# Kernel tuning notes

Hardware: AMD Instinct MI355X
Metric: run time of the kernel (lower is better)

## Reference

```python
import jax, jax.numpy as jnp
import numpy as np

EPS = 1e-5
K = 9
DILATION = 1

def bn(x, g, b, m, v):
    # x: (B,C,N,1), inference-mode BatchNorm2d with running stats
    sh = (1, -1, 1, 1)
    return (x - m.reshape(sh)) * (g.reshape(sh) / jnp.sqrt(v.reshape(sh) + EPS)) + b.reshape(sh)

def conv1x1(x, w, b):
    # w: (Cout, Cin), x: (B,Cin,N,1)
    return jnp.einsum('oc,bcnj->bonj', w, x) + b.reshape(1, -1, 1, 1)

def knn_idx(feat, k):
    # feat: (B,C,N) -> (B,N,k) indices of k nearest nodes (incl. self)
    xt = jnp.transpose(feat, (0, 2, 1))  # (B,N,C)
    x2 = jnp.sum(xt * xt, axis=-1)       # (B,N)
    dist = x2[:, :, None] - 2.0 * jnp.einsum('bnc,bmc->bnm', xt, xt) + x2[:, None, :]
    _, idx = jax.lax.top_k(-dist, k)
    return idx

def setup_inputs():
    key = jax.random.key(0)
    ks = jax.random.split(key, 24)
    B, C, H, W = 16, 256, 32, 32
    HID = 512
    def g(i, shape, s=1.0):
        return jax.random.normal(ks[i], shape, dtype=jnp.float32) * s
    def pos(i, shape):
        return jax.random.uniform(ks[i], shape, dtype=jnp.float32, minval=0.5, maxval=1.5)
    return {
        'x': g(0, (B, C, H, W)),
        'fc1_w': g(1, (C, C), 0.05), 'fc1_b': g(2, (C,), 0.05),
        'bn1_g': pos(3, (C,)), 'bn1_b': g(4, (C,), 0.1), 'bn1_m': g(5, (C,), 0.1), 'bn1_v': pos(6, (C,)),
        'gc_w': g(7, (HID, 2 * C), 0.05), 'gc_b': g(8, (HID,), 0.05),
        'gbn_g': pos(9, (HID,)), 'gbn_b': g(10, (HID,), 0.1), 'gbn_m': g(11, (HID,), 0.1), 'gbn_v': pos(12, (HID,)),
        'bn2_g': pos(13, (HID,)), 'bn2_b': g(14, (HID,), 0.1), 'bn2_m': g(15, (HID,), 0.1), 'bn2_v': pos(16, (HID,)),
        'fc2_w': g(17, (C, HID), 0.05), 'fc2_b': g(18, (C,), 0.05),
        'bn3_g': pos(19, (C,)), 'bn3_b': g(20, (C,), 0.1), 'bn3_m': g(21, (C,), 0.1), 'bn3_v': pos(22, (C,)),
    }

def reference(x, fc1_w, fc1_b, bn1_g, bn1_b, bn1_m, bn1_v,
              gc_w, gc_b, gbn_g, gbn_b, gbn_m, gbn_v,
              bn2_g, bn2_b, bn2_m, bn2_v,
              fc2_w, fc2_b, bn3_g, bn3_b, bn3_m, bn3_v):
    B, C, H, W = x.shape
    N = H * W
    x = x.reshape(B, C, N, 1)
    shortcut = x
    # fc1: 1x1 conv + BN
    h = bn(conv1x1(x, fc1_w, fc1_b), bn1_g, bn1_b, bn1_m, bn1_v)
    # DyGraphConv2d: dynamic dilated kNN graph over N nodes
    feat = h[..., 0]  # (B,C,N)
    idx = knn_idx(feat, K * DILATION)[:, :, ::DILATION]  # (B,N,K)
    # MRConv2d: max over neighbors of (x_j - x_i)
    x_j = jax.vmap(lambda f, i: f[:, i])(feat, idx)        # (B,C,N,K) gather
    diff_max = jnp.max(x_j - feat[:, :, :, None], axis=-1)  # (B,C,N)
    # interleave [x, max_diff] along channel dim -> (B, 2C, N, 1)
    m = jnp.stack([feat, diff_max], axis=2).reshape(B, 2 * C, N, 1)
    g = conv1x1(m, gc_w, gc_b)
    g = bn(g, gbn_g, gbn_b, gbn_m, gbn_v)  # BasicConv BN, act='None'
    # graph_conv Sequential: BN + GELU (erf, torch default)
    g = jax.nn.gelu(bn(g, bn2_g, bn2_b, bn2_m, bn2_v), approximate=False)
    # fc2 + residual (drop_path=0 -> identity)
    out = bn(conv1x1(g, fc2_w, fc2_b), bn3_g, bn3_b, bn3_m, bn3_v)
    return out + shortcut
```

## Files before the change

### kernel.cpp

```cpp
#include <hip/hip_runtime.h>
#include <hip/hip_bf16.h>
#include <stdint.h>

typedef unsigned long long u64;
typedef __hip_bfloat16 bf16;
typedef short s8v __attribute__((ext_vector_type(8)));
typedef short s4v __attribute__((ext_vector_type(4)));
typedef float f4v __attribute__((ext_vector_type(4)));

#define B_   16
#define C_   256
#define N_   1024
#define HID_ 512

__device__ __forceinline__ unsigned short f2b(float f) {
    unsigned u = __float_as_uint(f);
    unsigned r = (u + 0x7FFFu + ((u >> 16) & 1u)) >> 16;
    return (unsigned short)r;
}
__device__ __forceinline__ float b2f(unsigned short s) {
    return __uint_as_float(((unsigned)s) << 16);
}
__device__ __forceinline__ float ldIn(const void* p, long long i, int bf) {
    return bf ? b2f(((const unsigned short*)p)[i]) : ((const float*)p)[i];
}
__device__ __forceinline__ u64 shfl_xor_u64(u64 v, int m) {
    unsigned lo = (unsigned)v, hi = (unsigned)(v >> 32);
    lo = __shfl_xor(lo, m, 64);
    hi = __shfl_xor(hi, m, 64);
    return ((u64)hi << 32) | lo;
}

__global__ void prep_kernel(const void* xp,
    const void* fc1_b, const void* bn1_g, const void* bn1_b, const void* bn1_m, const void* bn1_v,
    const void* gc_b,  const void* gbn_g, const void* gbn_b, const void* gbn_m, const void* gbn_v,
    const void* bn2_g, const void* bn2_b, const void* bn2_m, const void* bn2_v,
    const void* fc2_b, const void* bn3_g, const void* bn3_b, const void* bn3_m, const void* bn3_v,
    int* flags, float* s1, float* t1, float* Sg, float* Tg, float* s3, float* t3,
    float* x2)
{
    __shared__ int sf;
    if (threadIdx.x == 0) {
        const unsigned short* u = (const unsigned short*)xp;
        int cnt = 0;
        for (int i = 0; i < 64; ++i) {
            int e = (u[2 * i] >> 7) & 0xFF;
            cnt += (e >= 87 && e <= 167);
        }
        int f = (cnt >= 48) ? 1 : 0;
        flags[0] = f;
        sf = f;
    }
    for (int i = threadIdx.x; i < B_ * N_; i += 512) x2[i] = 0.f;
    __syncthreads();
    int bf = sf;
    int i = threadIdx.x;
    if (i < 256) {
        float g = ldIn(bn1_g, i, bf), bb = ldIn(bn1_b, i, bf);
        float m = ldIn(bn1_m, i, bf), v  = ldIn(bn1_v, i, bf);
        float s = g / sqrtf(v + 1e-5f);
        s1[i] = s;
        t1[i] = (ldIn(fc1_b, i, bf) - m) * s + bb;

        float g3 = ldIn(bn3_g, i, bf), b3 = ldIn(bn3_b, i, bf);
        float m3 = ldIn(bn3_m, i, bf), v3 = ldIn(bn3_v, i, bf);
        float ss3 = g3 / sqrtf(v3 + 1e-5f);
        s3[i] = ss3;
        t3[i] = (ldIn(fc2_b, i, bf) - m3) * ss3 + b3;
    }
    if (i < 512) {
        float gg = ldIn(gbn_g, i, bf), gb = ldIn(gbn_b, i, bf);
        float gm = ldIn(gbn_m, i, bf), gv = ldIn(gbn_v, i, bf);
        float sg = gg / sqrtf(gv + 1e-5f);
        float g2 = ldIn(bn2_g, i, bf), b2 = ldIn(bn2_b, i, bf);
        float m2 = ldIn(bn2_m, i, bf), v2 = ldIn(bn2_v, i, bf);
        float s2 = g2 / sqrtf(v2 + 1e-5f);
        Sg[i] = sg * s2;
        Tg[i] = ((ldIn(gc_b, i, bf) - gm) * sg + gb - m2) * s2 + b2;
    }
}

__global__ __launch_bounds__(256)
void cast_weights(const void* w1, const void* wg, const void* w2,
                  short* W1h, short* W1l, short* Wgb, short* W2b,
                  const int* flags)
{
    int inf = flags[0];
    int i = blockIdx.x * 256 + threadIdx.x;
    if (i < 65536) {
        float f = ldIn(w1, i, inf);
        unsigned short h = f2b(f);
        W1h[i] = (short)h;
        W1l[i] = (short)f2b(f - b2f(h));
    } else if (i < 65536 + 262144) {
        int j = i - 65536;
        Wgb[j] = (short)f2b(ldIn(wg, j, inf));
    } else {
        int j = i - 327680;
        W2b[j] = (short)f2b(ldIn(w2, j, inf));
    }
}

__global__ __launch_bounds__(256)
void transpose_split_x(const void* __restrict__ X, short* __restrict__ xth,
                       short* __restrict__ xtl, const int* __restrict__ flags)
{
    __shared__ float tile[64][68];
    int inf = flags[0];
    int t = threadIdx.x;
    int n0 = blockIdx.x * 64, c0 = blockIdx.y * 64, b = blockIdx.z;

    #pragma unroll
    for (int rr = 0; rr < 4; ++rr) {
        int cl = (t >> 4) + rr * 16;
        int nl = (t & 15) * 4;
        long long g = ((long long)b * C_ + c0 + cl) * N_ + n0 + nl;
        if (inf) {
            s4v v = *(const s4v*)((const short*)X + g);
            tile[cl][nl + 0] = b2f((unsigned short)v[0]);
            tile[cl][nl + 1] = b2f((unsigned short)v[1]);
            tile[cl][nl + 2] = b2f((unsigned short)v[2]);
            tile[cl][nl + 3] = b2f((unsigned short)v[3]);
        } else {
            f4v v = *(const f4v*)((const float*)X + g);
            tile[cl][nl + 0] = v[0]; tile[cl][nl + 1] = v[1];
            tile[cl][nl + 2] = v[2]; tile[cl][nl + 3] = v[3];
        }
    }
    __syncthreads();

    int nl = t >> 2, cseg = t & 3;
    long long base = ((long long)((b << 10) + n0 + nl)) * C_ + c0 + cseg * 16;
    s8v h0, h1, l0, l1;
    #pragma unroll
    for (int cc = 0; cc < 16; ++cc) {
        float f = tile[cseg * 16 + cc][nl];
        unsigned short h = f2b(f);
        unsigned short l = f2b(f - b2f(h));
        if (cc < 8) { h0[cc] = (short)h; l0[cc] = (short)l; }
        else        { h1[cc - 8] = (short)h; l1[cc - 8] = (short)l; }
    }
    *(s8v*)(xth + base)     = h0;
    *(s8v*)(xth + base + 8) = h1;
    *(s8v*)(xtl + base)     = l0;
    *(s8v*)(xtl + base + 8) = l1;
}

__global__ __launch_bounds__(256)
void fc1_mfma(const short* __restrict__ W1h, const short* __restrict__ W1l,
              const short* __restrict__ xth, const short* __restrict__ xtl,
              const float* __restrict__ s1, const float* __restrict__ t1,
              float* __restrict__ Ft, short* __restrict__ Fhi,
              short* __restrict__ Flo, float* __restrict__ x2)
{
    __shared__ __align__(16) char ldsbuf[30720];
    short* Wh = (short*)(ldsbuf);
    short* Wl = (short*)(ldsbuf + 10240);
    short* Xh = (short*)(ldsbuf + 20480);
    short* Xl = (short*)(ldsbuf + 25600);

    int t = threadIdx.x;
    int n0 = blockIdx.x * 64, o0 = blockIdx.y * 128, b = blockIdx.z;
    int wv = t >> 6, ln15 = t & 15, quad = (t >> 4) & 3;

    f4v acc[8];
    #pragma unroll
    for (int i = 0; i < 8; ++i) acc[i] = 0.f;

    for (int kc = 0; kc < 8; ++kc) {
        __syncthreads();
        #pragma unroll
        for (int s = 0; s < 6; ++s) {
            int sid = t + s * 256;
            int row = sid >> 2, seg = sid & 3;
            const short* src;
            short* dst;
            if (row < 128)      { dst = &Wh[row * 40 + seg * 8];         src = W1h + (long long)(o0 + row) * C_; }
            else if (row < 256) { dst = &Wl[(row - 128) * 40 + seg * 8]; src = W1l + (long long)(o0 + row - 128) * C_; }
            else if (row < 320) { dst = &Xh[(row - 256) * 40 + seg * 8]; src = xth + ((long long)((b << 10) + n0 + row - 256)) * C_; }
            else                { dst = &Xl[(row - 320) * 40 + seg * 8]; src = xtl + ((long long)((b << 10) + n0 + row - 320)) * C_; }
            *(s8v*)dst = *(const s8v*)(src + kc * 32 + seg * 8);
        }
        __syncthreads();
        s8v xh8 = *(s8v*)&Xh[(wv * 16 + ln15) * 40 + quad * 8];
        s8v xl8 = *(s8v*)&Xl[(wv * 16 + ln15) * 40 + quad * 8];
        #pragma unroll
        for (int i = 0; i < 8; ++i) {
            s8v wh8 = *(s8v*)&Wh[(i * 16 + ln15) * 40 + quad * 8];
            s8v wl8 = *(s8v*)&Wl[(i * 16 + ln15) * 40 + quad * 8];
            acc[i] = __builtin_amdgcn_mfma_f32_16x16x32_bf16(wh8, xh8, acc[i], 0, 0, 0);
            acc[i] = __builtin_amdgcn_mfma_f32_16x16x32_bf16(wh8, xl8, acc[i], 0, 0, 0);
            acc[i] = __builtin_amdgcn_mfma_f32_16x16x32_bf16(wl8, xh8, acc[i], 0, 0, 0);
        }
    }

    int n = n0 + wv * 16 + ln15;
    long long nb = (long long)(b << 10) + n;
    float p2 = 0.f;
    #pragma unroll
    for (int i = 0; i < 8; ++i) {
        int ob = o0 + i * 16 + quad * 4;
        f4v f;
        s4v hi, lo;
        #pragma unroll
        for (int r = 0; r < 4; ++r) {
            float v = acc[i][r] * s1[ob + r] + t1[ob + r];
            f[r] = v;
            unsigned short h = f2b(v);
            hi[r] = (short)h;
            lo[r] = (short)f2b(v - b2f(h));
            p2 += v * v;
        }
        *(f4v*)(Ft  + nb * C_ + ob) = f;
        *(s4v*)(Fhi + nb * C_ + ob) = hi;
        *(s4v*)(Flo + nb * C_ + ob) = lo;
    }
    p2 += __shfl_xor(p2, 16, 64);
    p2 += __shfl_xor(p2, 32, 64);
    if (quad == 0) atomicAdd(&x2[nb], p2);
}

__global__ __launch_bounds__(256)
void gram_topk(const short* __restrict__ Fhi, const short* __restrict__ Flo,
               const float* __restrict__ x2, u64* __restrict__ Part)
{
    __shared__ __align__(16) char ldsbuf[31232];
    short* Ah  = (short*)(ldsbuf);
    short* Al  = (short*)(ldsbuf + 10240);
    short* Bh  = (short*)(ldsbuf + 20480);
    short* Bl  = (short*)(ldsbuf + 25600);
    float* x2s = (float*)(ldsbuf + 30720);
    u64*   mrg  = (u64*)(ldsbuf);
    u64*   mrg2 = (u64*)(ldsbuf + 20480);

    int t = threadIdx.x;
    int q0 = blockIdx.x * 64, mq = blockIdx.y, b = blockIdx.z;
    int wv = t >> 6, ln15 = t & 15, quad = (t >> 4) & 3;

    if (t < 128) x2s[t] = x2[(b << 10) + mq * 128 + t];

    f4v acc[8];
    #pragma unroll
    for (int i = 0; i < 8; ++i) acc[i] = 0.f;

    for (int kc = 0; kc < 8; ++kc) {
        __syncthreads();
        #pragma unroll
        for (int s = 0; s < 6; ++s) {
            int sid = t + s * 256;
            int row = sid >> 2, seg = sid & 3;
            const short* src;
            short* dst;
            int grow;
            if (row < 128)      { dst = &Ah[row * 40 + seg * 8];         grow = mq * 128 + row;       src = Fhi; }
            else if (row < 256) { dst = &Al[(row - 128) * 40 + seg * 8]; grow = mq * 128 + row - 128; src = Flo; }
            else if (row < 320) { dst = &Bh[(row - 256) * 40 + seg * 8]; grow = q0 + row - 256;       src = Fhi; }
            else                { dst = &Bl[(row - 320) * 40 + seg * 8]; grow = q0 + row - 320;       src = Flo; }
            *(s8v*)dst = *(const s8v*)(src + ((long long)((b << 10) + grow)) * C_ + kc * 32 + seg * 8);
        }
        __syncthreads();
        s8v qh = *(s8v*)&Bh[(wv * 16 + ln15) * 40 + quad * 8];
        s8v ql = *(s8v*)&Bl[(wv * 16 + ln15) * 40 + quad * 8];
        #pragma unroll
        for (int i = 0; i < 8; ++i) {
            s8v mh = *(s8v*)&Ah[(i * 16 + ln15) * 40 + quad * 8];
            s8v ml = *(s8v*)&Al[(i * 16 + ln15) * 40 + quad * 8];
            acc[i] = __builtin_amdgcn_mfma_f32_16x16x32_bf16(mh, qh, acc[i], 0, 0, 0);
            acc[i] = __builtin_amdgcn_mfma_f32_16x16x32_bf16(mh, ql, acc[i], 0, 0, 0);
            acc[i] = __builtin_amdgcn_mfma_f32_16x16x32_bf16(ml, qh, acc[i], 0, 0, 0);
        }
    }

    u64 l[9];
    #pragma unroll
    for (int i = 0; i < 9; ++i) l[i] = ~0ULL;
    #pragma unroll
    for (int i = 0; i < 8; ++i) {
        #pragma unroll
        for (int r = 0; r < 4; ++r) {
            int mloc = i * 16 + quad * 4 + r;
            float d = x2s[mloc] - 2.f * acc[i][r];
            unsigned u = __float_as_uint(d);
            u = (u & 0x80000000u) ? ~u : (u | 0x80000000u);
            u64 key = ((u64)u << 32) | (unsigned)(mq * 128 + mloc);
            if (key < l[8]) {
                u64 x = key;
                #pragma unroll
                for (int jj = 0; jj < 9; ++jj) {
                    u64 lo2 = l[jj] < x ? l[jj] : x;
                    u64 hi2 = l[jj] < x ? x : l[jj];
                    l[jj] = lo2; x = hi2;
                }
            }
        }
    }

    __syncthreads();
    {
        int qloc = wv * 16 + ln15;
        #pragma unroll
        for (int k = 0; k < 9; ++k) mrg[(qloc * 4 + quad) * 9 + k] = l[k];
    }
    __syncthreads();
    if (t < 128) {
        int r = t >> 1, pr = t & 1;
        const u64* LA = &mrg[(r * 4 + pr * 2) * 9];
        const u64* LB = LA + 9;
        int ia = 0, ib = 0;
        u64* Po = &mrg2[(r * 2 + pr) * 9];
        #pragma unroll
        for (int k = 0; k < 9; ++k) {
            u64 va = LA[ia], vb = LB[ib];
            bool ta = va < vb;
            Po[k] = ta ? va : vb;
            ia += ta; ib += !ta;
        }
    }
    __syncthreads();
    if (t < 64) {
        const u64* LA = &mrg2[(t * 2) * 9];
        const u64* LB = LA + 9;
        int ia = 0, ib = 0;
        u64* P = Part + (((long long)((b << 10) + q0 + t)) * 8 + mq) * 9;
        #pragma unroll
        for (int k = 0; k < 9; ++k) {
            u64 va = LA[ia], vb = LB[ib];
            bool ta = va < vb;
            P[k] = ta ? va : vb;
            ia += ta; ib += !ta;
        }
    }
}

__global__ __launch_bounds__(256)
void build_Mt(const float* __restrict__ Ft, const u64* __restrict__ Part,
              short* __restrict__ Mt)
{
    int t = threadIdx.x;
    int wv = t >> 6, lane = t & 63;
    int n = blockIdx.x * 4 + wv;
    int b = blockIdx.y;
    long long nb = (long long)(b << 10) + n;

    const u64* L = Part + nb * 72 + (long long)(lane & 7) * 9;
    u64 l[9];
    #pragma unroll
    for (int k = 0; k < 9; ++k) l[k] = L[k];
    #pragma unroll
    for (int s = 1; s <= 4; s <<= 1) {
        u64 p[9];
        #pragma unroll
        for (int k = 0; k < 9; ++k) p[k] = shfl_xor_u64(l[k], s);
        #pragma unroll
        for (int k = 0; k < 9; ++k) {
            u64 x = p[k];
            if (x < l[8]) {
                #pragma unroll
                for (int jj = 0; jj < 9; ++jj) {
                    u64 lo2 = l[jj] < x ? l[jj] : x;
                    u64 hi2 = l[jj] < x ? x : l[jj];
                    l[jj] = lo2; x = hi2;
                }
            }
        }
    }

    int c0 = lane * 4;
    f4v f = *(const f4v*)(Ft + nb * C_ + c0);
    f4v mx = {-3.4e38f, -3.4e38f, -3.4e38f, -3.4e38f};
    #pragma unroll
    for (int k = 0; k < 9; ++k) {
        int id = (int)(l[k] & 0xFFFFFFFFu);
        f4v g = *(const f4v*)(Ft + ((long long)(b << 10) + id) * C_ + c0);
        mx[0] = fmaxf(mx[0], g[0]); mx[1] = fmaxf(mx[1], g[1]);
        mx[2] = fmaxf(mx[2], g[2]); mx[3] = fmaxf(mx[3], g[3]);
    }
    s8v m8;
    #pragma unroll
    for (int r = 0; r < 4; ++r) {
        m8[2 * r]     = (short)f2b(f[r]);
        m8[2 * r + 1] = (short)f2b(mx[r] - f[r]);
    }
    *(s8v*)(Mt + nb * (2 * C_) + 2 * c0) = m8;
}

template<int EPI>
__global__ __launch_bounds__(256)
void mfma_gemm(const short* __restrict__ A, const short* __restrict__ Bm,
               void* __restrict__ Out, const float* __restrict__ scale,
               const float* __restrict__ bias, const void* __restrict__ resid,
               const int* __restrict__ flags, int K, int Odim)
{
    __shared__ __align__(16) short As[128 * 40];
    __shared__ __align__(16) short Bs[64 * 40];

    int t = threadIdx.x, b = blockIdx.z;
    int n0 = blockIdx.x * 64, o0 = blockIdx.y * 128;
    int wv = t >> 6, ln15 = t & 15, quad = (t >> 4) & 3;

    f4v acc[8];
    #pragma unroll
    for (int i = 0; i < 8; ++i) acc[i] = 0.f;

    int nkc = K >> 5;
    for (int kc = 0; kc < nkc; ++kc) {
        __syncthreads();
        #pragma unroll
        for (int s = 0; s < 3; ++s) {
            int sid = t + s * 256;
            int row = sid >> 2, seg = sid & 3;
            if (row < 128)
                *(s8v*)&As[row * 40 + seg * 8] =
                    *(const s8v*)(A + (long long)(o0 + row) * K + kc * 32 + seg * 8);
            else
                *(s8v*)&Bs[(row - 128) * 40 + seg * 8] =
                    *(const s8v*)(Bm + ((long long)((b << 10) + n0 + row - 128)) * K + kc * 32 + seg * 8);
        }
        __syncthreads();
        s8v bf = *(s8v*)&Bs[(wv * 16 + ln15) * 40 + quad * 8];
        #pragma unroll
        for (int i = 0; i < 8; ++i) {
            s8v a = *(s8v*)&As[(i * 16 + ln15) * 40 + quad * 8];
            acc[i] = __builtin_amdgcn_mfma_f32_16x16x32_bf16(a, bf, acc[i], 0, 0, 0);
        }
    }

    int inf = flags[0];
    int n = n0 + wv * 16 + ln15;
    #pragma unroll
    for (int i = 0; i < 8; ++i) {
        int ob = o0 + i * 16 + quad * 4;
        if (EPI == 0) {
            s4v g;
            #pragma unroll
            for (int r = 0; r < 4; ++r) {
                float val = acc[i][r] * scale[ob + r] + bias[ob + r];
                val = 0.5f * val * (1.0f + erff(val * 0.70710678118654752f));
                g[r] = (short)f2b(val);
            }
            *(s4v*)((short*)Out + ((long long)((b << 10) + n)) * Odim + ob) = g;
        } else {
            #pragma unroll
            for (int r = 0; r < 4; ++r) {
                int o = ob + r;
                long long oi = ((long long)b * Odim + o) * N_ + n;
                ((float*)Out)[oi] = acc[i][r] * scale[o] + bias[o] + ldIn(resid, oi, inf);
            }
        }
    }
}

extern "C" void kernel_launch(void* const* d_in, const int* in_sizes, int n_in,
                              void* d_out, int out_size, void* d_ws, size_t ws_size,
                              hipStream_t stream)
{
    const void* p[23];
    if (n_in >= 23 && in_sizes[0] != 4194304 && in_sizes[22] == 4194304) {
        const int amap[23] = {
            22, 13, 12, 1, 0, 2, 3,
            21, 20, 17, 16, 18, 19,
            5, 4, 6, 7,
            15, 14, 9, 8, 10, 11 };
        for (int i = 0; i < 23; ++i) p[i] = d_in[amap[i]];
    } else {
        for (int i = 0; i < 23; ++i) p[i] = d_in[i];
    }

    const void* x     = p[0];
    const void* fc1_w = p[1];
    const void* fc1_b = p[2];
    const void* bn1_g = p[3];
    const void* bn1_b = p[4];
    const void* bn1_m = p[5];
    const void* bn1_v = p[6];
    const void* gc_w  = p[7];
    const void* gc_b  = p[8];
    const void* gbn_g = p[9];
    const void* gbn_b = p[10];
    const void* gbn_m = p[11];
    const void* gbn_v = p[12];
    const void* bn2_g = p[13];
    const void* bn2_b = p[14];
    const void* bn2_m = p[15];
    const void* bn2_v = p[16];
    const void* fc2_w = p[17];
    const void* fc2_b = p[18];
    const void* bn3_g = p[19];
    const void* bn3_b = p[20];
    const void* bn3_m = p[21];
    const void* bn3_v = p[22];

    char* ws = (char*)d_ws;
    size_t off = 0;
    int*   flags = (int*)ws;
    float* s1 = (float*)(ws + 256);
    float* t1 = s1 + 256;
    float* s3 = t1 + 256;
    float* t3 = s3 + 256;
    float* Sg = t3 + 256;
    float* Tg = Sg + 512;
    off = 16384;
    short* W1h   = (short*)(ws + off); off += (size_t)C_ * C_ * 2;
    short* W1l   = (short*)(ws + off); off += (size_t)C_ * C_ * 2;
    short* Wgb   = (short*)(ws + off); off += (size_t)HID_ * 2 * C_ * 2;
    short* W2b   = (short*)(ws + off); off += (size_t)C_ * HID_ * 2;
    short* xth   = (short*)(ws + off); off += (size_t)B_ * N_ * C_ * 2;
    short* xtl   = (short*)(ws + off); off += (size_t)B_ * N_ * C_ * 2;
    float* Ft    = (float*)(ws + off); off += (size_t)B_ * N_ * C_ * 4;
    short* Fhi   = (short*)(ws + off); off += (size_t)B_ * N_ * C_ * 2;
    short* Flo   = (short*)(ws + off); off += (size_t)B_ * N_ * C_ * 2;
    float* x2    = (float*)(ws + off); off += (size_t)B_ * N_ * 4;
    u64*   Part  = (u64*)  (ws + off); off += (size_t)B_ * N_ * 8 * 9 * 8;
    short* Mt    = (short*)(ws + off); off += (size_t)B_ * N_ * 2 * C_ * 2;
    short* Gt    = (short*)(ws + off); off += (size_t)B_ * N_ * HID_ * 2;

    prep_kernel<<<1, 512, 0, stream>>>(x,
        fc1_b, bn1_g, bn1_b, bn1_m, bn1_v,
        gc_b, gbn_g, gbn_b, gbn_m, gbn_v,
        bn2_g, bn2_b, bn2_m, bn2_v,
        fc2_b, bn3_g, bn3_b, bn3_m, bn3_v,
        flags, s1, t1, Sg, Tg, s3, t3, x2);

    cast_weights<<<1792, 256, 0, stream>>>(fc1_w, gc_w, fc2_w,
                                           W1h, W1l, Wgb, W2b, flags);

    transpose_split_x<<<dim3(16, 4, 16), 256, 0, stream>>>(x, xth, xtl, flags);

    fc1_mfma<<<dim3(16, 2, 16), 256, 0, stream>>>(
        W1h, W1l, xth, xtl, s1, t1, Ft, Fhi, Flo, x2);

    gram_topk<<<dim3(16, 8, 16), 256, 0, stream>>>(Fhi, Flo, x2, Part);

    build_Mt<<<dim3(256, 16), 256, 0, stream>>>(Ft, Part, Mt);

    mfma_gemm<0><<<dim3(16, 4, 16), 256, 0, stream>>>(
        Wgb, Mt, Gt, Sg, Tg, nullptr, flags, 2 * C_, HID_);

    mfma_gemm<1><<<dim3(16, 2, 16), 256, 0, stream>>>(
        W2b, Gt, d_out, s3, t3, x, flags, HID_, C_);
}
```

Before: 301.9 us.

## Double-buffer weight tiles via direct global-to-LDS loads and register-resident B operand

In fc1 and gram_topk, the per-wave B operand (activation/query rows) is now loaded once from global memory into registers for all K chunks rather than being staged through LDS. The A operand (weights/candidate rows) is copied with global_load_lds straight into a double-buffered, unpadded LDS layout, and the next chunk is prefetched while MFMAs consume the current one. This removes one of the two barriers per iteration and the VGPR round-trip on the staging path, so loads can overlap compute. The costs are higher register pressure from 16 s8v registers per thread, and possible LDS bank conflicts because the row padding has been removed.

```diff
diff --git a/kernel.cpp b/kernel.cpp
--- a/kernel.cpp
+++ b/kernel.cpp
@@ -12,6 +12,11 @@
 #define C_   256
 #define N_   1024
 #define HID_ 512
+
+#define GLD16(g, l)                                                         \
+    __builtin_amdgcn_global_load_lds(                                       \
+        (const __attribute__((address_space(1))) void*)(g),                 \
+        (__attribute__((address_space(3))) void*)(l), 16, 0, 0)
 
 __device__ __forceinline__ unsigned short f2b(float f) {
     unsigned u = __float_as_uint(f);
@@ -153,46 +158,62 @@
               float* __restrict__ Ft, short* __restrict__ Fhi,
               short* __restrict__ Flo, float* __restrict__ x2)
 {
-    __shared__ __align__(16) char ldsbuf[30720];
-    short* Wh = (short*)(ldsbuf);
-    short* Wl = (short*)(ldsbuf + 10240);
-    short* Xh = (short*)(ldsbuf + 20480);
-    short* Xl = (short*)(ldsbuf + 25600);
+    __shared__ __align__(16) char ldsbuf[32768];
 
     int t = threadIdx.x;
     int n0 = blockIdx.x * 64, o0 = blockIdx.y * 128, b = blockIdx.z;
-    int wv = t >> 6, ln15 = t & 15, quad = (t >> 4) & 3;
+    int wv = t >> 6, lane = t & 63, ln15 = t & 15, quad = (t >> 4) & 3;
+
+    const short* gAh = W1h + (long long)(o0 + wv * 32 + (lane >> 2)) * C_ + (lane & 3) * 8;
+    const short* gAl = W1l + (long long)(o0 + wv * 32 + (lane >> 2)) * C_ + (lane & 3) * 8;
+    short* lH0 = (short*)(ldsbuf)           + wv * 32 * 32;
+    short* lL0 = (short*)(ldsbuf + 8192)    + wv * 32 * 32;
+    short* lH1 = (short*)(ldsbuf + 16384)   + wv * 32 * 32;
+    short* lL1 = (short*)(ldsbuf + 24576)   + wv * 32 * 32;
+
+#define FC1_STAGE(kc_, bi_) do {                                              \
+        short* dh = (bi_) ? lH1 : lH0;                                        \
+        short* dl = (bi_) ? lL1 : lL0;                                        \
+        GLD16(gAh + (kc_) * 32,            dh);                               \
+        GLD16(gAh + (kc_) * 32 + 16 * C_,  dh + 16 * 32);                     \
+        GLD16(gAl + (kc_) * 32,            dl);                               \
+        GLD16(gAl + (kc_) * 32 + 16 * C_,  dl + 16 * 32);                     \
+    } while (0)
+
+    FC1_STAGE(0, 0);
+
+    s8v xh[8], xl[8];
+    {
+        long long xoff = (long long)((b << 10) + n0 + wv * 16 + ln15) * C_ + quad * 8;
+        #pragma unroll
+        for (int kc = 0; kc < 8; ++kc) {
+            xh[kc] = *(const s8v*)(xth + xoff + kc * 32);
+            xl[kc] = *(const s8v*)(xtl + xoff + kc * 32);
+        }
+    }
 
     f4v acc[8];
     #pragma unroll
     for (int i = 0; i < 8; ++i) acc[i] = 0.f;
 
+    __syncthreads();
+
+    #pragma unroll
     for (int kc = 0; kc < 8; ++kc) {
+        if (kc < 7) FC1_STAGE(kc + 1, (kc + 1) & 1);
+        const short* Ah_c = (const short*)(ldsbuf + (kc & 1) * 16384);
+        const short* Al_c = Ah_c + 4096;
+        #pragma unroll
+        for (int i = 0; i < 8; ++i) {
+            s8v wh8 = *(const s8v*)&Ah_c[(i * 16 + ln15) * 32 + quad * 8];
+            s8v wl8 = *(const s8v*)&Al_c[(i * 16 + ln15) * 32 + quad * 8];
+            acc[i] = __builtin_amdgcn_mfma_f32_16x16x32_bf16(wh8, xh[kc], acc[i], 0, 0, 0);
+            acc[i] = __builtin_amdgcn_mfma_f32_16x16x32_bf16(wh8, xl[kc], acc[i], 0, 0, 0);
+            acc[i] = __builtin_amdgcn_mfma_f32_16x16x32_bf16(wl8, xh[kc], acc[i], 0, 0, 0);
+        }
         __syncthreads();
-        #pragma unroll
-        for (int s = 0; s < 6; ++s) {
-            int sid = t + s * 256;
-            int row = sid >> 2, seg = sid & 3;
-            const short* src;
-            short* dst;
-            if (row < 128)      { dst = &Wh[row * 40 + seg * 8];         src = W1h + (long long)(o0 + row) * C_; }
-            else if (row < 256) { dst = &Wl[(row - 128) * 40 + seg * 8]; src = W1l + (long long)(o0 + row - 128) * C_; }
-            else if (row < 320) { dst = &Xh[(row - 256) * 40 + seg * 8]; src = xth + ((long long)((b << 10) + n0 + row - 256)) * C_; }
-            else                { dst = &Xl[(row - 320) * 40 + seg * 8]; src = xtl + ((long long)((b << 10) + n0 + row - 320)) * C_; }
-            *(s8v*)dst = *(const s8v*)(src + kc * 32 + seg * 8);
-        }
-        __syncthreads();
-        s8v xh8 = *(s8v*)&Xh[(wv * 16 + ln15) * 40 + quad * 8];
-        s8v xl8 = *(s8v*)&Xl[(wv * 16 + ln15) * 40 + quad * 8];
-        #pragma unroll
-        for (int i = 0; i < 8; ++i) {
-            s8v wh8 = *(s8v*)&Wh[(i * 16 + ln15) * 40 + quad * 8];
-            s8v wl8 = *(s8v*)&Wl[(i * 16 + ln15) * 40 + quad * 8];
-            acc[i] = __builtin_amdgcn_mfma_f32_16x16x32_bf16(wh8, xh8, acc[i], 0, 0, 0);
-            acc[i] = __builtin_amdgcn_mfma_f32_16x16x32_bf16(wh8, xl8, acc[i], 0, 0, 0);
-            acc[i] = __builtin_amdgcn_mfma_f32_16x16x32_bf16(wl8, xh8, acc[i], 0, 0, 0);
-        }
-    }
+    }
+#undef FC1_STAGE
 
     int n = n0 + wv * 16 + ln15;
     long long nb = (long long)(b << 10) + n;
@@ -224,52 +245,67 @@
 void gram_topk(const short* __restrict__ Fhi, const short* __restrict__ Flo,
                const float* __restrict__ x2, u64* __restrict__ Part)
 {
-    __shared__ __align__(16) char ldsbuf[31232];
-    short* Ah  = (short*)(ldsbuf);
-    short* Al  = (short*)(ldsbuf + 10240);
-    short* Bh  = (short*)(ldsbuf + 20480);
-    short* Bl  = (short*)(ldsbuf + 25600);
-    float* x2s = (float*)(ldsbuf + 30720);
+    __shared__ __align__(16) char ldsbuf[33280];
+    float* x2s = (float*)(ldsbuf + 32768);
     u64*   mrg  = (u64*)(ldsbuf);
     u64*   mrg2 = (u64*)(ldsbuf + 20480);
 
     int t = threadIdx.x;
     int q0 = blockIdx.x * 64, mq = blockIdx.y, b = blockIdx.z;
-    int wv = t >> 6, ln15 = t & 15, quad = (t >> 4) & 3;
+    int wv = t >> 6, lane = t & 63, ln15 = t & 15, quad = (t >> 4) & 3;
+
+    const short* gAh = Fhi + (long long)((b << 10) + mq * 128 + wv * 32 + (lane >> 2)) * C_ + (lane & 3) * 8;
+    const short* gAl = Flo + (long long)((b << 10) + mq * 128 + wv * 32 + (lane >> 2)) * C_ + (lane & 3) * 8;
+    short* lH0 = (short*)(ldsbuf)           + wv * 32 * 32;
+    short* lL0 = (short*)(ldsbuf + 8192)    + wv * 32 * 32;
+    short* lH1 = (short*)(ldsbuf + 16384)   + wv * 32 * 32;
+    short* lL1 = (short*)(ldsbuf + 24576)   + wv * 32 * 32;
+
+#define GRAM_STAGE(kc_, bi_) do {                                             \
+        short* dh = (bi_) ? lH1 : lH0;                                        \
+        short* dl = (bi_) ? lL1 : lL0;                                        \
+        GLD16(gAh + (kc_) * 32,            dh);                               \
+        GLD16(gAh + (kc_) * 32 + 16 * C_,  dh + 16 * 32);                     \
+        GLD16(gAl + (kc_) * 32,            dl);                               \
+        GLD16(gAl + (kc_) * 32 + 16 * C_,  dl + 16 * 32);                     \
+    } while (0)
+
+    GRAM_STAGE(0, 0);
 
     if (t < 128) x2s[t] = x2[(b << 10) + mq * 128 + t];
 
+    s8v qh[8], ql[8];
+    {
+        long long qoff = (long long)((b << 10) + q0 + wv * 16 + ln15) * C_ + quad * 8;
+        #pragma unroll
+        for (int kc = 0; kc < 8; ++kc) {
+            qh[kc] = *(const s8v*)(Fhi + qoff + kc * 32);
+            ql[kc] = *(const s8v*)(Flo + qoff + kc * 32);
+        }
+    }
+
     f4v acc[8];
     #pragma unroll
     for (int i = 0; i < 8; ++i) acc[i] = 0.f;
 
+    __syncthreads();
+
+    #pragma unroll
     for (int kc = 0; kc < 8; ++kc) {
+        if (kc < 7) GRAM_STAGE(kc + 1, (kc + 1) & 1);
+        const short* Ah_c = (const short*)(ldsbuf + (kc & 1) * 16384);
+        const short* Al_c = Ah_c + 4096;
+        #pragma unroll
+        for (int i = 0; i < 8; ++i) {
+            s8v mh = *(const s8v*)&Ah_c[(i * 16 + ln15) * 32 + quad * 8];
+            s8v ml = *(const s8v*)&Al_c[(i * 16 + ln15) * 32 + quad * 8];
+            acc[i] = __builtin_amdgcn_mfma_f32_16x16x32_bf16(mh, qh[kc], acc[i], 0, 0, 0);
+            acc[i] = __builtin_amdgcn_mfma_f32_16x16x32_bf16(mh, ql[kc], acc[i], 0, 0, 0);
+            acc[i] = __builtin_amdgcn_mfma_f32_16x16x32_bf16(ml, qh[kc], acc[i], 0, 0, 0);
+        }
         __syncthreads();
-        #pragma unroll
-        for (int s = 0; s < 6; ++s) {
-            int sid = t + s * 256;
-            int row = sid >> 2, seg = sid & 3;
-            const short* src;
-            short* dst;
-            int grow;
-            if (row < 128)      { dst = &Ah[row * 40 + seg * 8];         grow = mq * 128 + row;       src = Fhi; }
-            else if (row < 256) { dst = &Al[(row - 128) * 40 + seg * 8]; grow = mq * 128 + row - 128; src = Flo; }
-            else if (row < 320) { dst = &Bh[(row - 256) * 40 + seg * 8]; grow = q0 + row - 256;       src = Fhi; }
-            else                { dst = &Bl[(row - 320) * 40 + seg * 8]; grow = q0 + row - 320;       src = Flo; }
-            *(s8v*)dst = *(const s8v*)(src + ((long long)((b << 10) + grow)) * C_ + kc * 32 + seg * 8);
-        }
-        __syncthreads();
-        s8v qh = *(s8v*)&Bh[(wv * 16 + ln15) * 40 + quad * 8];
-        s8v ql = *(s8v*)&Bl[(wv * 16 + ln15) * 40 + quad * 8];
-        #pragma unroll
-        for (int i = 0; i < 8; ++i) {
-            s8v mh = *(s8v*)&Ah[(i * 16 + ln15) * 40 + quad * 8];
-            s8v ml = *(s8v*)&Al[(i * 16 + ln15) * 40 + quad * 8];
-            acc[i] = __builtin_amdgcn_mfma_f32_16x16x32_bf16(mh, qh, acc[i], 0, 0, 0);
-            acc[i] = __builtin_amdgcn_mfma_f32_16x16x32_bf16(mh, ql, acc[i], 0, 0, 0);
-            acc[i] = __builtin_amdgcn_mfma_f32_16x16x32_bf16(ml, qh, acc[i], 0, 0, 0);
-        }
-    }
+    }
+#undef GRAM_STAGE
 
     u64 l[9];
     #pragma unroll
```

After: 290.8 us. 3.7% less time.
